# Performance work log

Measured on AMD Instinct MI355X. Metric: run time of the kernel, lower is better.

Reference implementation:

```python
import jax, jax.numpy as jnp
import numpy as np

BN_EPS = 1e-5

def _conv(x, w, b, pad):
    # x: [B,C,H,W], w: [O,I,kh,kw] -> [B,O,H,W]
    y = jax.lax.conv_general_dilated(x, w, window_strides=(1, 1),
                                     padding=[(pad, pad), (pad, pad)],
                                     dimension_numbers=("NCHW", "OIHW", "NCHW"))
    return y + b[None, :, None, None]

def setup_inputs() -> dict:
    key = jax.random.key(0)
    ks = jax.random.split(key, 5)
    B, Cin, H, W = 2, 256, 80, 80
    Ck, Cv, Cout = 128, 256, 256
    std = 0.02  # matches torch normal_(0, 0.02) init
    return {
        "x": jax.random.normal(ks[0], (B, Cin, H, W), jnp.float32),
        "wk": std * jax.random.normal(ks[1], (Ck, Cin, 1, 1), jnp.float32),
        "bk": jnp.zeros((Ck,), jnp.float32),
        "gamma": jnp.ones((Ck,), jnp.float32),
        "beta": jnp.zeros((Ck,), jnp.float32),
        "rmean": jnp.zeros((Ck,), jnp.float32),
        "rvar": jnp.ones((Ck,), jnp.float32),
        "wv": std * jax.random.normal(ks[2], (Cv, Cin, 3, 3), jnp.float32),
        "bv": jnp.zeros((Cv,), jnp.float32),
        "ww": std * jax.random.normal(ks[3], (Cout, Cv, 1, 1), jnp.float32),
        "bw": jnp.zeros((Cout,), jnp.float32),
    }

def reference(x, wk, bk, gamma, beta, rmean, rvar, wv, bv, ww, bw):
    B, Cin, H, W = x.shape
    Ck, Cv = wk.shape[0], wv.shape[0]
    N = H * W

    # f_key == f_query (shared module): 1x1 conv + BatchNorm (inference stats)
    kq = _conv(x, wk, bk, pad=0)                      # [B,Ck,H,W]
    inv = gamma / jnp.sqrt(rvar + BN_EPS)
    kq = kq * inv[None, :, None, None] + (beta - rmean * inv)[None, :, None, None]
    kq = kq.reshape(B, Ck, N)                          # key layout [B,Ck,N]

    # f_value: 3x3 conv
    value = _conv(x, wv, bv, pad=1).reshape(B, Cv, N)  # [B,Cv,N]

    # sim_map = query^T @ key -> [B,N,N], full softmax over last dim
    sim = jnp.einsum("bcn,bcm->bnm", kq, kq)
    sim = jax.nn.softmax(sim, axis=-1)

    # context = sim @ value^T -> [B,N,Cv] -> [B,Cv,H,W]
    ctx = jnp.einsum("bnm,bcm->bcn", sim, value).reshape(B, Cv, H, W)

    out = _conv(ctx, ww, bw, pad=0) + x                # residual
    return out
```

## Files before the change

kernel.cpp:

```cpp
#include <hip/hip_runtime.h>
#include <math.h>

#define NB   2
#define CIN  256
#define IMH  80
#define IMW  80
#define NPIX (IMH*IMW)
#define CK   128
#define CVC  256
#define COUTC 256
#define BN_EPS 1e-5f
#define HP   82
#define WP   82
#define NMC  (NPIX / 64)
#define LOG2E 1.4426950408889634f
#define M0L  28.853900817779268f

typedef short sx8 __attribute__((ext_vector_type(8)));
typedef short sx4 __attribute__((ext_vector_type(4)));
typedef float f32x4 __attribute__((ext_vector_type(4)));

__device__ __forceinline__ short f2bf(float f) {
    unsigned u = __builtin_bit_cast(unsigned, f);
    u += 0x7fffu + ((u >> 16) & 1u);
    return (short)(u >> 16);
}
__device__ __forceinline__ float bf2f(short s) {
    unsigned u = ((unsigned)(unsigned short)s) << 16;
    return __builtin_bit_cast(float, u);
}
__device__ __forceinline__ int pk_bf16(float a, float b) {
    unsigned ua = __builtin_bit_cast(unsigned, a) + 0x8000u;
    unsigned ub = __builtin_bit_cast(unsigned, b) + 0x8000u;
    return __builtin_amdgcn_perm(ub, ua, 0x07060302);
}

__global__ __launch_bounds__(256) void pad_kernel(const float* __restrict__ x,
                                                  short* __restrict__ xpad)
{
    __shared__ short T[64][258];
    const int tid = threadIdx.x;
    const int n0  = blockIdx.x * 64;
    const int b   = blockIdx.y;
    const float* xb = x + (size_t)b * CIN * NPIX;

    #pragma unroll 4
    for (int i = 0; i < 64; ++i) {
        int e = tid + i * 256;
        int pix = e & 63, c = e >> 6;
        T[pix][c] = f2bf(xb[(size_t)c * NPIX + n0 + pix]);
    }
    __syncthreads();
    #pragma unroll
    for (int i = 0; i < 8; ++i) {
        int e   = tid + i * 256;
        int pix = e >> 5;
        int cp  = (e & 31) * 8;
        int np  = n0 + pix;
        int hp  = np / IMW + 1, wp = np % IMW + 1;
        sx8 v = *(const sx8*)&T[pix][cp];
        *(sx8*)&xpad[(((size_t)b * HP + hp) * WP + wp) * CIN + cp] = v;
    }
}

__global__ __launch_bounds__(256) void wvt_kernel(const float* __restrict__ wv,
                                                  short* __restrict__ wvt)
{
    int idx = blockIdx.x * 256 + threadIdx.x;
    int tap = idx >> 16;
    int cv  = (idx >> 8) & 255;
    int c   = idx & 255;
    wvt[idx] = f2bf(wv[((size_t)cv * CIN + c) * 9 + tap]);
}

__global__ __launch_bounds__(256) void wwb_kernel(const float* __restrict__ ww,
                                                  short* __restrict__ wwb)
{
    int idx = blockIdx.x * 256 + threadIdx.x;
    wwb[idx] = f2bf(ww[idx]);
}

__global__ __launch_bounds__(256) void wkb_kernel(
    const float* __restrict__ wk, const float* __restrict__ bk,
    const float* __restrict__ gamma, const float* __restrict__ beta,
    const float* __restrict__ rmean, const float* __restrict__ rvar,
    short* __restrict__ wkb, float* __restrict__ bias2)
{
    int idx = blockIdx.x * 256 + threadIdx.x;
    int ck = idx >> 8;
    float inv = gamma[ck] * rsqrtf(rvar[ck] + BN_EPS);
    wkb[idx] = f2bf(wk[idx] * inv);
    if (idx < CK) {
        float invi = gamma[idx] * rsqrtf(rvar[idx] + BN_EPS);
        bias2[idx] = (bk[idx] - rmean[idx]) * invi + beta[idx];
    }
}

__global__ __launch_bounds__(256) void kq_kernel(
    const short* __restrict__ xpad, const short* __restrict__ wkb,
    const float* __restrict__ bias2, short* __restrict__ kqT)
{
    __shared__ short T[64][136];
    const int tid  = threadIdx.x;
    const int wid  = tid >> 6;
    const int lane = tid & 63;
    const int l15  = lane & 15;
    const int quad = lane >> 4;
    const int n0 = blockIdx.x * 64;
    const int b  = blockIdx.y;
    const short* xb = xpad + (size_t)b * HP * WP * CIN;
    const int ck0 = wid * 32;

    const short* brow[4];
    #pragma unroll
    for (int nt = 0; nt < 4; ++nt) {
        int n = n0 + nt * 16 + l15;
        int hp = n / IMW + 1, wp = n % IMW + 1;
        brow[nt] = xb + ((size_t)hp * WP + wp) * CIN;
    }

    f32x4 acc[2][4];
    #pragma unroll
    for (int at = 0; at < 2; ++at)
        #pragma unroll
        for (int nt = 0; nt < 4; ++nt)
            acc[at][nt] = (f32x4){0.f, 0.f, 0.f, 0.f};

    for (int kc = 0; kc < CIN / 32; ++kc) {
        sx8 af0 = *(const sx8*)&wkb[(size_t)(ck0 + l15) * CIN + kc * 32 + quad * 8];
        sx8 af1 = *(const sx8*)&wkb[(size_t)(ck0 + 16 + l15) * CIN + kc * 32 + quad * 8];
        #pragma unroll
        for (int nt = 0; nt < 4; ++nt) {
            sx8 bf = *(const sx8*)&brow[nt][kc * 32 + quad * 8];
            acc[0][nt] = __builtin_amdgcn_mfma_f32_16x16x32_bf16(af0, bf, acc[0][nt], 0, 0, 0);
            acc[1][nt] = __builtin_amdgcn_mfma_f32_16x16x32_bf16(af1, bf, acc[1][nt], 0, 0, 0);
        }
    }

    #pragma unroll
    for (int at = 0; at < 2; ++at) {
        f32x4 b4 = *(const f32x4*)&bias2[ck0 + at * 16 + quad * 4];
        #pragma unroll
        for (int nt = 0; nt < 4; ++nt)
            #pragma unroll
            for (int r = 0; r < 4; ++r)
                T[nt * 16 + l15][ck0 + at * 16 + quad * 4 + r] = f2bf(acc[at][nt][r] + b4[r]);
    }
    __syncthreads();
    #pragma unroll
    for (int it = 0; it < 4; ++it) {
        int e = tid + it * 256;
        int row = e >> 4, c8 = (e & 15) * 8;
        *(sx8*)&kqT[((size_t)b * NPIX + n0 + row) * CK + c8] = *(const sx8*)&T[row][c8];
    }
}

#define CSTRIDE 36
__global__ __launch_bounds__(256) void conv3_kernel(
    const short* __restrict__ xpad, const short* __restrict__ wvt,
    const float* __restrict__ bv, short* __restrict__ valF)
{
    __shared__ __align__(16) short Xs[6 * 18 * CSTRIDE];

    const int tid  = threadIdx.x;
    const int wid  = tid >> 6;
    const int lane = tid & 63;
    const int l15  = lane & 15;
    const int quad = lane >> 4;

    const int rowT = blockIdx.x / 5, colT = blockIdx.x % 5;
    const int h0 = rowT * 4, w0 = colT * 16;
    const int cv0 = blockIdx.y * 64 + wid * 16;
    const int b   = blockIdx.z;

    const short* xb = xpad + (size_t)b * HP * WP * CIN;

    f32x4 acc[4];
    #pragma unroll
    for (int r = 0; r < 4; ++r) acc[r] = (f32x4){0.f, 0.f, 0.f, 0.f};

    for (int cc = 0; cc < CIN / 32; ++cc) {
        __syncthreads();
        #pragma unroll
        for (int i = 0; i < 2; ++i) {
            int e = tid + i * 256;
            if (e < 432) {
                int rc = e >> 2, l4 = e & 3;
                int row = rc / 18, col = rc % 18;
                sx8 v = *(const sx8*)&xb[(((size_t)(h0 + row)) * WP + (w0 + col)) * CIN + cc * 32 + l4 * 8];
                *(sx8*)&Xs[rc * CSTRIDE + l4 * 8] = v;
            }
        }
        __syncthreads();

        #pragma unroll
        for (int dw = 0; dw < 3; ++dw) {
            sx8 Bf[6];
            #pragma unroll
            for (int rr = 0; rr < 6; ++rr)
                Bf[rr] = *(const sx8*)&Xs[(rr * 18 + l15 + dw) * CSTRIDE + quad * 8];
            #pragma unroll
            for (int dh = 0; dh < 3; ++dh) {
                int tap = dh * 3 + dw;
                sx8 Af = *(const sx8*)&wvt[((size_t)(tap * 256 + cv0 + l15)) * CIN + cc * 32 + quad * 8];
                #pragma unroll
                for (int r = 0; r < 4; ++r)
                    acc[r] = __builtin_amdgcn_mfma_f32_16x16x32_bf16(Af, Bf[r + dh], acc[r], 0, 0, 0);
            }
        }
    }

    f32x4 bvv = *(const f32x4*)&bv[cv0 + quad * 4];
    const int cvt = cv0 >> 4;
    #pragma unroll
    for (int r = 0; r < 4; ++r) {
        int n  = (h0 + r) * IMW + w0 + l15;
        int mc = n >> 6, s2 = (n >> 5) & 1, qm = (n >> 3) & 3, mi = n & 7;
        size_t base = ((((size_t)(b * NMC + mc) * 16 + cvt) * 2 + s2) * 4 + qm) * 128;
        #pragma unroll
        for (int reg = 0; reg < 4; ++reg)
            valF[base + (quad * 4 + reg) * 8 + mi] = f2bf(acc[r][reg] + bvv[reg]);
    }
}

#define TQ 64
#define TK 64
#define KS_LD 132
#define PS_LD 72

template<int SP>
__global__ __launch_bounds__(512) void attn_kernel(
    const short* __restrict__ kqT, const short* __restrict__ valF,
    short* __restrict__ opart, float* __restrict__ lpart)
{
    constexpr int NCc  = NPIX / SP / 64;
    constexpr int SPSH = (SP == 4) ? 3 : 2;

    __shared__ __align__(16) short Ks[TK][KS_LD];
    __shared__ __align__(16) short Pb[TQ][PS_LD];
    __shared__ float lqs[2][64];

    const int tid  = threadIdx.x;
    const int wid  = tid >> 6;
    const int lane = tid & 63;
    const int l15  = lane & 15;
    const int quad = lane >> 4;
    const int qw   = wid & 3;
    const int mh   = wid >> 2;

    const int blk = blockIdx.x;
    const int b   = blk & 1;
    const int sp  = (blk >> 1) & (SP - 1);
    const int n0  = (blk >> SPSH) * TQ;
    const int mb  = sp * (NPIX / SP);

    const short* kqb = kqT + (size_t)b * NPIX * CK;
    const short* vbase = valF + ((size_t)(b * NMC + sp * NCc) * 16 + wid * 2) * 1024
                              + (size_t)lane * 8;

    const int srow = tid >> 4;
    const int sc8  = (tid & 15) * 8;

    sx8 qf[4];
    #pragma unroll
    for (int s = 0; s < 4; ++s)
        qf[s] = *(const sx8*)&kqb[(size_t)(n0 + qw * 16 + l15) * CK + s * 32 + quad * 8];

    sx8 kreg[2];
    #pragma unroll
    for (int p = 0; p < 2; ++p)
        kreg[p] = *(const sx8*)&kqb[(size_t)(mb + srow + p * 32) * CK + sc8];
    #pragma unroll
    for (int p = 0; p < 2; ++p)
        *(sx8*)&Ks[srow + p * 32][sc8] = kreg[p];

    sx8 vreg[4];
    #pragma unroll
    for (int ct = 0; ct < 2; ++ct)
        #pragma unroll
        for (int s2 = 0; s2 < 2; ++s2)
            vreg[ct * 2 + s2] = *(const sx8*)&vbase[ct * 1024 + s2 * 512];

    float lq = 0.f;
    f32x4 acc[4][2];
    #pragma unroll
    for (int qt = 0; qt < 4; ++qt)
        #pragma unroll
        for (int ct = 0; ct < 2; ++ct)
            acc[qt][ct] = (f32x4){0.f, 0.f, 0.f, 0.f};

    __syncthreads();

    for (int i = 0; i < NCc; ++i) {
        if (i + 1 < NCc) {
            #pragma unroll
            for (int p = 0; p < 2; ++p)
                kreg[p] = *(const sx8*)&kqb[(size_t)(mb + (i + 1) * TK + srow + p * 32) * CK + sc8];
        }

        f32x4 st[2];
        #pragma unroll
        for (int t2 = 0; t2 < 2; ++t2) st[t2] = (f32x4){0.f, 0.f, 0.f, 0.f};
        #pragma unroll
        for (int s = 0; s < 4; ++s) {
            sx8 af[2];
            #pragma unroll
            for (int t2 = 0; t2 < 2; ++t2)
                af[t2] = *(const sx8*)&Ks[mh * 32 + t2 * 16 + l15][s * 32 + quad * 8];
            #pragma unroll
            for (int t2 = 0; t2 < 2; ++t2)
                st[t2] = __builtin_amdgcn_mfma_f32_16x16x32_bf16(af[t2], qf[s], st[t2], 0, 0, 0);
        }

        __syncthreads();

        #pragma unroll
        for (int t2 = 0; t2 < 2; ++t2)
            #pragma unroll
            for (int r = 0; r < 4; ++r)
                st[t2][r] = exp2f(fmaf(st[t2][r], LOG2E, -M0L));

        if (i + 1 < NCc) {
            #pragma unroll
            for (int p = 0; p < 2; ++p)
                *(sx8*)&Ks[srow + p * 32][sc8] = kreg[p];
        }

        #pragma unroll
        for (int t2 = 0; t2 < 2; ++t2) {
            int2 pw;
            pw.x = pk_bf16(st[t2][0], st[t2][1]);
            pw.y = pk_bf16(st[t2][2], st[t2][3]);
            *(int2*)&Pb[qw * 16 + l15][mh * 32 + t2 * 16 + quad * 4] = pw;
        }

        lq += (st[0][0] + st[0][1]) + (st[0][2] + st[0][3])
            + (st[1][0] + st[1][1]) + (st[1][2] + st[1][3]);

        __syncthreads();

        #pragma unroll
        for (int s2 = 0; s2 < 2; ++s2) {
            sx8 pa[4];
            #pragma unroll
            for (int qt = 0; qt < 4; ++qt)
                pa[qt] = *(const sx8*)&Pb[qt * 16 + l15][s2 * 32 + quad * 8];
            #pragma unroll
            for (int ct = 0; ct < 2; ++ct) {
                #pragma unroll
                for (int qt = 0; qt < 4; ++qt)
                    acc[qt][ct] = __builtin_amdgcn_mfma_f32_16x16x32_bf16(pa[qt], vreg[ct * 2 + s2], acc[qt][ct], 0, 0, 0);
            }
        }

        if (i + 1 < NCc) {
            #pragma unroll
            for (int ct = 0; ct < 2; ++ct)
                #pragma unroll
                for (int s2 = 0; s2 < 2; ++s2)
                    vreg[ct * 2 + s2] = *(const sx8*)&vbase[(size_t)(i + 1) * 16384 + ct * 1024 + s2 * 512];
        }
    }

    lq += __shfl_xor(lq, 16);
    lq += __shfl_xor(lq, 32);
    if (quad == 0)
        lqs[mh][qw * 16 + l15] = lq;

    size_t obase = (size_t)(sp * NB + b) * NPIX + n0;
    #pragma unroll
    for (int qt = 0; qt < 4; ++qt)
        #pragma unroll
        for (int ct = 0; ct < 2; ++ct) {
            int cv = wid * 32 + ct * 16 + l15;
            #pragma unroll
            for (int r = 0; r < 4; ++r)
                opart[(obase + qt * 16 + quad * 4 + r) * CVC + cv] = f2bf(acc[qt][ct][r]);
        }

    __syncthreads();
    if (tid < 64)
        lpart[obase + tid] = lqs[0][tid] + lqs[1][tid];
}

#define BS_LD 40
template<int SP>
__global__ __launch_bounds__(256) void out_kernel(
    const short* __restrict__ opart, const float* __restrict__ lpart,
    const short* __restrict__ wwb, const float* __restrict__ bw,
    const float* __restrict__ x, float* __restrict__ out)
{
    __shared__ __align__(16) short Bs[64][BS_LD];
    __shared__ float rinvs[64];

    const int tid  = threadIdx.x;
    const int wid  = tid >> 6;
    const int lane = tid & 63;
    const int l15  = lane & 15;
    const int quad = lane >> 4;

    const int n0  = blockIdx.x * 64;
    const int co0 = blockIdx.y * 64 + wid * 16;
    const int b   = blockIdx.z;

    if (tid < 64) {
        int n = n0 + tid;
        float ls = 0.f;
        #pragma unroll
        for (int s = 0; s < SP; ++s)
            ls += lpart[(size_t)(s * NB + b) * NPIX + n];
        rinvs[tid] = 1.f / ls;
    }

    const int srow = tid >> 2;
    const int sc8  = (tid & 3) * 8;
    const short* op0 = opart + ((size_t)b * NPIX + n0 + srow) * CVC + sc8;
    constexpr size_t SSTR = (size_t)NB * NPIX * CVC;

    f32x4 acc[4];
    #pragma unroll
    for (int nt = 0; nt < 4; ++nt) acc[nt] = (f32x4){0.f, 0.f, 0.f, 0.f};

    for (int cc = 0; cc < CVC / 32; ++cc) {
        __syncthreads();
        {
            float ri = rinvs[srow];
            float sacc[8] = {0.f, 0.f, 0.f, 0.f, 0.f, 0.f, 0.f, 0.f};
            #pragma unroll
            for (int s = 0; s < SP; ++s) {
                sx8 a = *(const sx8*)&op0[s * SSTR + cc * 32];
                #pragma unroll
                for (int j = 0; j < 8; ++j)
                    sacc[j] += bf2f(a[j]);
            }
            sx8 o;
            #pragma unroll
            for (int j = 0; j < 8; ++j)
                o[j] = f2bf(sacc[j] * ri);
            *(sx8*)&Bs[srow][sc8] = o;
        }
        __syncthreads();
        sx8 af = *(const sx8*)&wwb[(size_t)(co0 + l15) * CVC + cc * 32 + quad * 8];
        #pragma unroll
        for (int nt = 0; nt < 4; ++nt) {
            sx8 bf = *(const sx8*)&Bs[nt * 16 + l15][quad * 8];
            acc[nt] = __builtin_amdgcn_mfma_f32_16x16x32_bf16(af, bf, acc[nt], 0, 0, 0);
        }
    }

    f32x4 bv4 = *(const f32x4*)&bw[co0 + quad * 4];
    #pragma unroll
    for (int nt = 0; nt < 4; ++nt) {
        #pragma unroll
        for (int r = 0; r < 4; ++r) {
            int co = co0 + quad * 4 + r;
            int n  = n0 + nt * 16 + l15;
            size_t gi = ((size_t)b * COUTC + co) * NPIX + n;
            out[gi] = acc[nt][r] + bv4[r] + x[gi];
        }
    }
}

extern "C" void kernel_launch(void* const* d_in, const int* in_sizes, int n_in,
                              void* d_out, int out_size, void* d_ws, size_t ws_size,
                              hipStream_t stream)
{
    const float* x     = (const float*)d_in[0];
    const float* wk    = (const float*)d_in[1];
    const float* bk    = (const float*)d_in[2];
    const float* gamma = (const float*)d_in[3];
    const float* beta  = (const float*)d_in[4];
    const float* rmean = (const float*)d_in[5];
    const float* rvar  = (const float*)d_in[6];
    const float* wv    = (const float*)d_in[7];
    const float* bv    = (const float*)d_in[8];
    const float* ww    = (const float*)d_in[9];
    const float* bw    = (const float*)d_in[10];
    float* out = (float*)d_out;

    const size_t perSplit = (size_t)NB * NPIX * CVC;
    const size_t persistShorts = (size_t)COUTC * CVC + (size_t)CK * CIN
                               + (size_t)NB * NPIX * CK + (size_t)NB * NPIX * CVC;
    const size_t need4 = 2ull * (4ull * perSplit + persistShorts)
                       + 4ull * (CK + 4ull * NB * NPIX);
    const int SPL = (ws_size >= need4) ? 4 : 2;

    short* opart = (short*)d_ws;
    short* xpad  = opart;
    short* wvt   = xpad + (size_t)NB * HP * WP * CIN;
    short* wwb   = opart + (size_t)SPL * perSplit;
    short* wkb   = wwb  + (size_t)COUTC * CVC;
    short* kqT   = wkb  + (size_t)CK * CIN;
    short* valF  = kqT  + (size_t)NB * NPIX * CK;
    float* bias2 = (float*)(valF + perSplit);
    float* lpart = bias2 + CK;

    hipMemsetAsync(xpad, 0, (size_t)NB * HP * WP * CIN * sizeof(short), stream);

    pad_kernel   <<<dim3(NPIX/64, NB),          256, 0, stream>>>(x, xpad);
    wvt_kernel   <<<(9*CVC*CIN)/256,            256, 0, stream>>>(wv, wvt);
    wwb_kernel   <<<(COUTC*CVC)/256,            256, 0, stream>>>(ww, wwb);
    wkb_kernel   <<<(CK*CIN)/256,               256, 0, stream>>>(wk, bk, gamma, beta, rmean, rvar, wkb, bias2);
    kq_kernel    <<<dim3(NPIX/64, NB),          256, 0, stream>>>(xpad, wkb, bias2, kqT);
    conv3_kernel <<<dim3(100, CVC/64,      NB), 256, 0, stream>>>(xpad, wvt, bv, valF);

    if (SPL == 4) {
        attn_kernel<4> <<<NB * 4 * (NPIX / TQ), 512, 0, stream>>>(kqT, valF, opart, lpart);
        out_kernel<4>  <<<dim3(100, COUTC/64, NB), 256, 0, stream>>>(opart, lpart, wwb, bw, x, out);
    } else {
        attn_kernel<2> <<<NB * 2 * (NPIX / TQ), 512, 0, stream>>>(kqT, valF, opart, lpart);
        out_kernel<2>  <<<dim3(100, COUTC/64, NB), 256, 0, stream>>>(opart, lpart, wwb, bw, x, out);
    }
}
```

Baseline: 243.3 us.

## Double-buffer LDS staging and widen blocks in conv3 and output projection kernels

The 3x3 value conv and the output 1x1 projection kernels now prefetch the next channel chunk into registers while MFMAs run on the current LDS buffer, using a two-slot shared buffer with one barrier per iteration. Blocks grow to 512 threads covering 128 output channels each, so the staged input tile is shared by twice as many waves and the grid halves. This aims to hide global load latency and cut redundant input staging, at the cost of fewer blocks in flight and more register pressure.

Result: no change. 243.3 us (+0.0%).

```diff
diff --git a/kernel.cpp b/kernel.cpp
--- a/kernel.cpp
+++ b/kernel.cpp
@@ -156,11 +156,11 @@
 }
 
 #define CSTRIDE 36
-__global__ __launch_bounds__(256) void conv3_kernel(
+__global__ __launch_bounds__(512) void conv3_kernel(
     const short* __restrict__ xpad, const short* __restrict__ wvt,
     const float* __restrict__ bv, short* __restrict__ valF)
 {
-    __shared__ __align__(16) short Xs[6 * 18 * CSTRIDE];
+    __shared__ __align__(16) short Xs[2][6 * 18 * CSTRIDE];
 
     const int tid  = threadIdx.x;
     const int wid  = tid >> 6;
@@ -170,35 +170,39 @@
 
     const int rowT = blockIdx.x / 5, colT = blockIdx.x % 5;
     const int h0 = rowT * 4, w0 = colT * 16;
-    const int cv0 = blockIdx.y * 64 + wid * 16;
+    const int cv0 = blockIdx.y * 128 + wid * 16;
     const int b   = blockIdx.z;
 
     const short* xb = xpad + (size_t)b * HP * WP * CIN;
 
+    const int rc  = tid >> 2, l4 = tid & 3;
+    const int row = rc / 18, col = rc % 18;
+    const bool sv = (tid < 432);
+    const short* sptr = &xb[(((size_t)(h0 + row)) * WP + (w0 + col)) * CIN + l4 * 8];
+    const int sdst = rc * CSTRIDE + l4 * 8;
+
     f32x4 acc[4];
     #pragma unroll
     for (int r = 0; r < 4; ++r) acc[r] = (f32x4){0.f, 0.f, 0.f, 0.f};
 
+    sx8 v = {};
+    if (sv) {
+        v = *(const sx8*)&sptr[0];
+        *(sx8*)&Xs[0][sdst] = v;
+    }
+    __syncthreads();
+
     for (int cc = 0; cc < CIN / 32; ++cc) {
-        __syncthreads();
-        #pragma unroll
-        for (int i = 0; i < 2; ++i) {
-            int e = tid + i * 256;
-            if (e < 432) {
-                int rc = e >> 2, l4 = e & 3;
-                int row = rc / 18, col = rc % 18;
-                sx8 v = *(const sx8*)&xb[(((size_t)(h0 + row)) * WP + (w0 + col)) * CIN + cc * 32 + l4 * 8];
-                *(sx8*)&Xs[rc * CSTRIDE + l4 * 8] = v;
-            }
-        }
-        __syncthreads();
+        const int cur = cc & 1;
+        if (cc + 1 < CIN / 32 && sv)
+            v = *(const sx8*)&sptr[(cc + 1) * 32];
 
         #pragma unroll
         for (int dw = 0; dw < 3; ++dw) {
             sx8 Bf[6];
             #pragma unroll
             for (int rr = 0; rr < 6; ++rr)
-                Bf[rr] = *(const sx8*)&Xs[(rr * 18 + l15 + dw) * CSTRIDE + quad * 8];
+                Bf[rr] = *(const sx8*)&Xs[cur][(rr * 18 + l15 + dw) * CSTRIDE + quad * 8];
             #pragma unroll
             for (int dh = 0; dh < 3; ++dh) {
                 int tap = dh * 3 + dw;
@@ -208,6 +212,10 @@
                     acc[r] = __builtin_amdgcn_mfma_f32_16x16x32_bf16(Af, Bf[r + dh], acc[r], 0, 0, 0);
             }
         }
+
+        if (cc + 1 < CIN / 32 && sv)
+            *(sx8*)&Xs[cur ^ 1][sdst] = v;
+        __syncthreads();
     }
 
     f32x4 bvv = *(const f32x4*)&bv[cv0 + quad * 4];
@@ -385,12 +393,12 @@
 
 #define BS_LD 40
 template<int SP>
-__global__ __launch_bounds__(256) void out_kernel(
+__global__ __launch_bounds__(512) void out_kernel(
     const short* __restrict__ opart, const float* __restrict__ lpart,
     const short* __restrict__ wwb, const float* __restrict__ bw,
     const float* __restrict__ x, float* __restrict__ out)
 {
-    __shared__ __align__(16) short Bs[64][BS_LD];
+    __shared__ __align__(16) short Bs[2][64][BS_LD];
     __shared__ float rinvs[64];
 
     const int tid  = threadIdx.x;
@@ -400,7 +408,7 @@
     const int quad = lane >> 4;
 
     const int n0  = blockIdx.x * 64;
-    const int co0 = blockIdx.y * 64 + wid * 16;
+    const int co0 = blockIdx.y * 128 + wid * 16;
     const int b   = blockIdx.z;
 
     if (tid < 64) {
@@ -416,36 +424,65 @@
     const int sc8  = (tid & 3) * 8;
     const short* op0 = opart + ((size_t)b * NPIX + n0 + srow) * CVC + sc8;
     constexpr size_t SSTR = (size_t)NB * NPIX * CVC;
+    const bool sv = (tid < 256);
+
+    __syncthreads();
+
+    if (sv) {
+        float ri = rinvs[srow];
+        float sacc[8] = {0.f, 0.f, 0.f, 0.f, 0.f, 0.f, 0.f, 0.f};
+        #pragma unroll
+        for (int s = 0; s < SP; ++s) {
+            sx8 a = *(const sx8*)&op0[s * SSTR];
+            #pragma unroll
+            for (int j = 0; j < 8; ++j)
+                sacc[j] += bf2f(a[j]);
+        }
+        sx8 o;
+        #pragma unroll
+        for (int j = 0; j < 8; ++j)
+            o[j] = f2bf(sacc[j] * ri);
+        *(sx8*)&Bs[0][srow][sc8] = o;
+    }
+    __syncthreads();
 
     f32x4 acc[4];
     #pragma unroll
     for (int nt = 0; nt < 4; ++nt) acc[nt] = (f32x4){0.f, 0.f, 0.f, 0.f};
 
     for (int cc = 0; cc < CVC / 32; ++cc) {
-        __syncthreads();
-        {
+        const int cur = cc & 1;
+        const bool st = (cc + 1 < CVC / 32) && sv;
+
+        sx8 a[SP];
+        if (st) {
+            #pragma unroll
+            for (int s = 0; s < SP; ++s)
+                a[s] = *(const sx8*)&op0[s * SSTR + (cc + 1) * 32];
+        }
+
+        sx8 af = *(const sx8*)&wwb[(size_t)(co0 + l15) * CVC + cc * 32 + quad * 8];
+        #pragma unroll
+        for (int nt = 0; nt < 4; ++nt) {
+            sx8 bf = *(const sx8*)&Bs[cur][nt * 16 + l15][quad * 8];
+            acc[nt] = __builtin_amdgcn_mfma_f32_16x16x32_bf16(af, bf, acc[nt], 0, 0, 0);
+        }
+
+        if (st) {
             float ri = rinvs[srow];
             float sacc[8] = {0.f, 0.f, 0.f, 0.f, 0.f, 0.f, 0.f, 0.f};
             #pragma unroll
-            for (int s = 0; s < SP; ++s) {
-                sx8 a = *(const sx8*)&op0[s * SSTR + cc * 32];
+            for (int s = 0; s < SP; ++s)
                 #pragma unroll
                 for (int j = 0; j < 8; ++j)
-                    sacc[j] += bf2f(a[j]);
-            }
+                    sacc[j] += bf2f(a[s][j]);
             sx8 o;
             #pragma unroll
             for (int j = 0; j < 8; ++j)
                 o[j] = f2bf(sacc[j] * ri);
-            *(sx8*)&Bs[srow][sc8] = o;
+            *(sx8*)&Bs[cur ^ 1][srow][sc8] = o;
         }
         __syncthreads();
-        sx8 af = *(const sx8*)&wwb[(size_t)(co0 + l15) * CVC + cc * 32 + quad * 8];
-        #pragma unroll
-        for (int nt = 0; nt < 4; ++nt) {
-            sx8 bf = *(const sx8*)&Bs[nt * 16 + l15][quad * 8];
-            acc[nt] = __builtin_amdgcn_mfma_f32_16x16x32_bf16(af, bf, acc[nt], 0, 0, 0);
-        }
     }
 
     f32x4 bv4 = *(const f32x4*)&bw[co0 + quad * 4];
@@ -502,13 +539,13 @@
     wwb_kernel   <<<(COUTC*CVC)/256,            256, 0, stream>>>(ww, wwb);
     wkb_kernel   <<<(CK*CIN)/256,               256, 0, stream>>>(wk, bk, gamma, beta, rmean, rvar, wkb, bias2);
     kq_kernel    <<<dim3(NPIX/64, NB),          256, 0, stream>>>(xpad, wkb, bias2, kqT);
-    conv3_kernel <<<dim3(100, CVC/64,      NB), 256, 0, stream>>>(xpad, wvt, bv, valF);
+    conv3_kernel <<<dim3(100, CVC/128,     NB), 512, 0, stream>>>(xpad, wvt, bv, valF);
 
     if (SPL == 4) {
         attn_kernel<4> <<<NB * 4 * (NPIX / TQ), 512, 0, stream>>>(kqT, valF, opart, lpart);
-        out_kernel<4>  <<<dim3(100, COUTC/64, NB), 256, 0, stream>>>(opart, lpart, wwb, bw, x, out);
+        out_kernel<4>  <<<dim3(100, COUTC/128, NB), 512, 0, stream>>>(opart, lpart, wwb, bw, x, out);
     } else {
         attn_kernel<2> <<<NB * 2 * (NPIX / TQ), 512, 0, stream>>>(kqT, valF, opart, lpart);
-        out_kernel<2>  <<<dim3(100, COUTC/64, NB), 256, 0, stream>>>(opart, lpart, wwb, bw, x, out);
-    }
-}
+        out_kernel<2>  <<<dim3(100, COUTC/128, NB), 512, 0, stream>>>(opart, lpart, wwb, bw, x, out);
+    }
+}
```
